# Performance work log

Hardware: AMD Instinct MI355X
Metric: run time of the kernel (lower is better)

The kernel has to match this reference:

```python
import jax, jax.numpy as jnp
from jax import lax
import numpy as np

EPS = 4e-3            # geoopt float32 ball boundary eps
MAXNORM = 1.0 - EPS   # c = 1 Poincare ball


def _norm(x):
    return jnp.sqrt(jnp.maximum(jnp.sum(x * x, axis=-1, keepdims=True), 1e-15))


def expmap0(u):
    n = _norm(u)
    return jnp.tanh(n) * u / n


def projx(x):
    n = _norm(x)
    return jnp.where(n > MAXNORM, x * (MAXNORM / n), x)


def mobius_add(x, y):
    x2 = jnp.sum(x * x, -1, keepdims=True)
    y2 = jnp.sum(y * y, -1, keepdims=True)
    xy = jnp.sum(x * y, -1, keepdims=True)
    num = (1.0 + 2.0 * xy + y2) * x + (1.0 - x2) * y
    den = 1.0 + 2.0 * xy + x2 * y2
    return num / jnp.maximum(den, 1e-15)


def mamba_layer(x, inW, convW, convb, xpW, dtW, dtb, A_log, Dp, outW):
    # x: [B,T,H]; inW: [2*Din,H]; convW: [Din,K]; xpW: [R+2N,Din]; dtW: [Din,R]
    B, T, H = x.shape
    Din, N = A_log.shape
    K = convW.shape[-1]
    R = dtW.shape[-1]
    xz = jnp.einsum('bth,dh->btd', x, inW)              # [B,T,2*Din]
    xr, z = jnp.split(xz, 2, axis=-1)
    xc = lax.conv_general_dilated(jnp.transpose(xr, (0, 2, 1)), convW[:, None, :],
                                  (1,), [(K - 1, 0)], feature_group_count=Din)
    u = jax.nn.silu(jnp.transpose(xc + convb[None, :, None], (0, 2, 1)))  # [B,T,Din]
    x_dbl = jnp.einsum('btd,ed->bte', u, xpW)           # [B,T,R+2N]
    dt_r, Bm, Cm = x_dbl[..., :R], x_dbl[..., R:R + N], x_dbl[..., R + N:]
    dt = jax.nn.softplus(jnp.einsum('btr,dr->btd', dt_r, dtW) + dtb)      # [B,T,Din]
    A = -jnp.exp(A_log)                                 # [Din,N]
    dA = jnp.exp(dt[..., None] * A)                     # [B,T,Din,N]
    dBu = dt[..., None] * Bm[:, :, None, :] * u[..., None]

    def step(h, ins):
        dA_t, dBu_t, C_t = ins
        h = dA_t * h + dBu_t                            # [B,Din,N]
        return h, jnp.einsum('bdn,bn->bd', h, C_t)

    h0 = jnp.zeros((B, Din, N), x.dtype)
    _, ys = lax.scan(step, h0, (jnp.moveaxis(dA, 1, 0), jnp.moveaxis(dBu, 1, 0), jnp.moveaxis(Cm, 1, 0)))
    y = jnp.moveaxis(ys, 0, 1) + Dp * u                 # [B,T,Din]
    return jnp.einsum('btd,hd->bth', y * jax.nn.silu(z), outW)


def _encode(xs, inp_W, inp_b, in_proj_W, conv_W, conv_b, xproj_W, dt_W, dt_b, A_log, D_skip, out_W, outp_W, outp_b):
    # xs: [4,B,T,1]; params carry leading branch dim 4, then layer dim 3
    def branch(x, iW, ib, ipW, cW, cb, xpW, dW, db, Al, Dp, oW, opW, opb):
        h = jnp.einsum('bti,hi->bth', x, iW) + ib
        for l in range(ipW.shape[0]):
            h = mamba_layer(h, ipW[l], cW[l], cb[l], xpW[l], dW[l], db[l], Al[l], Dp[l], oW[l])
        return jnp.tanh(jnp.einsum('bth,eh->bte', h, opW) + opb)
    return jax.vmap(branch)(xs, inp_W, inp_b, in_proj_W, conv_W, conv_b, xproj_W, dt_W, dt_b, A_log, D_skip, out_W, outp_W, outp_b)


def setup_inputs() -> dict:
    key = jax.random.key(0)
    ks = jax.random.split(key, 24)
    Br, B, T, H, Din, N, K, R, E, L = 4, 32, 1024, 64, 128, 16, 4, 4, 32, 3

    def rn(k, shape, s=0.05):
        return jax.random.normal(k, shape, jnp.float32) * s

    A_init = jnp.log(jnp.arange(1, N + 1, dtype=jnp.float32))
    return {
        'trend': jax.random.normal(ks[0], (B, T, 1), jnp.float32),
        'seasonal_weekly': jax.random.normal(ks[1], (B, T, 1), jnp.float32),
        'seasonal_daily': jax.random.normal(ks[2], (B, T, 1), jnp.float32),
        'residual': jax.random.normal(ks[3], (B, T, 1), jnp.float32),
        'inp_W': rn(ks[4], (Br, H, 1), 0.5),
        'inp_b': rn(ks[5], (Br, H)),
        'in_proj_W': rn(ks[6], (Br, L, 2 * Din, H)),
        'conv_W': rn(ks[7], (Br, L, Din, K), 0.2),
        'conv_b': rn(ks[8], (Br, L, Din)),
        'xproj_W': rn(ks[9], (Br, L, R + 2 * N, Din)),
        'dt_W': rn(ks[10], (Br, L, Din, R), 0.2),
        'dt_b': rn(ks[11], (Br, L, Din), 0.5) - 4.0,  # softplus(dt_b) small
        'A_log': jnp.tile(A_init, (Br, L, Din, 1)) + rn(ks[12], (Br, L, Din, N), 0.01),
        'D_skip': jnp.ones((Br, L, Din), jnp.float32) + rn(ks[13], (Br, L, Din), 0.01),
        'out_W': rn(ks[14], (Br, L, H, Din)),
        'outp_W': rn(ks[15], (Br, E, H)),
        'outp_b': rn(ks[16], (Br, E)),
    }


def reference(trend, seasonal_weekly, seasonal_daily, residual, inp_W, inp_b, in_proj_W, conv_W, conv_b, xproj_W, dt_W, dt_b, A_log, D_skip, out_W, outp_W, outp_b):
    xs = jnp.stack([trend, seasonal_weekly, seasonal_daily, residual], 0)  # [4,B,T,1]
    z = _encode(xs, inp_W, inp_b, in_proj_W, conv_W, conv_b, xproj_W, dt_W, dt_b, A_log, D_skip, out_W, outp_W, outp_b)  # [4,B,T,E]
    zh = projx(expmap0(z))
    t, w, d, r = zh[0], zh[1], zh[2], zh[3]
    comb = projx(mobius_add(mobius_add(t, mobius_add(w, d)), r))
    # stacked [trend_h, weekly_h, daily_h, residual_h, combined_h]
    return jnp.stack([t, w, d, r, comb], 0)
```

## Files before the change

### kernel.cpp

```cpp
#include <hip/hip_runtime.h>
#include <math.h>

#define TT 1024
#define DIN 128
#define HH 64
#define NN 16
#define EE 32
#define LL 3
#define BB 32

__device__ __forceinline__ float siluf(float x) { return x / (1.f + __expf(-x)); }

typedef __attribute__((ext_vector_type(8))) short bf16x8;
typedef __attribute__((ext_vector_type(4))) float f32x4;

__device__ __forceinline__ void split2(float x, ushort& hi, ushort& lo) {
  unsigned u = __float_as_uint(x);
  hi = (ushort)(u >> 16);
  float rem = x - __uint_as_float((u >> 16) << 16);
  lo = (ushort)(__float_as_uint(rem) >> 16);
}

#define WXZ_N 196608
#define WXD_N 73728
#define WOUT_N 98304

__global__ __launch_bounds__(256) void k_presplit(
    const float* __restrict__ iprojW, const float* __restrict__ xprojW,
    const float* __restrict__ outW,
    ushort* __restrict__ WxzH, ushort* __restrict__ WxzL,
    ushort* __restrict__ WxdH, ushort* __restrict__ WxdL,
    ushort* __restrict__ WoH, ushort* __restrict__ WoL) {
  int idx = blockIdx.x * 256 + threadIdx.x;
  if (idx < WXZ_N) {
    ushort h, l;
    split2(iprojW[idx], h, l);
    WxzH[idx] = h; WxzL[idx] = l;
  }
  if (idx < WXD_N) {
    int k = idx & 127, r = (idx >> 7) % 48, bl = idx / (48 * 128);
    float v = (r < 36) ? xprojW[((size_t)(bl * 36 + r)) * 128 + k] : 0.f;
    ushort h, l;
    split2(v, h, l);
    WxdH[idx] = h; WxdL[idx] = l;
  }
  if (idx < WOUT_N) {
    ushort h, l;
    split2(outW[idx], h, l);
    WoH[idx] = h; WoL[idx] = l;
  }
}

__global__ __launch_bounds__(256) void k_xz(
    const float* __restrict__ x0, const float* __restrict__ x1,
    const float* __restrict__ x2, const float* __restrict__ x3,
    const float* __restrict__ h, const ushort* __restrict__ WH,
    const ushort* __restrict__ WL,
    const float* __restrict__ inpW, const float* __restrict__ inpb,
    float* __restrict__ xr, float* __restrict__ zb, int br0, int l) {
  __shared__ __align__(16) ushort Hh[64][72], Hl[64][72];
  const int tid = threadIdx.x;
  const int b  = blockIdx.y;
  const int t0 = blockIdx.x * 64;
  const int br = br0 + (b >> 5);
  const float* Hg = h + ((size_t)b * TT + t0) * HH;
  {
    const int row = tid >> 2, c0 = (tid & 3) * 16;
    float xv = 0.f;
    if (l == 0) {
      int bb = b & 31;
      const float* xp = (br == 0) ? x0 : (br == 1) ? x1 : (br == 2) ? x2 : x3;
      xv = xp[bb * TT + t0 + row];
    }
    #pragma unroll
    for (int q = 0; q < 4; ++q) {
      float4 hv;
      if (l == 0) {
        float4 w4 = *(const float4*)(inpW + br * HH + c0 + q * 4);
        float4 b4 = *(const float4*)(inpb + br * HH + c0 + q * 4);
        hv.x = xv * w4.x + b4.x; hv.y = xv * w4.y + b4.y;
        hv.z = xv * w4.z + b4.z; hv.w = xv * w4.w + b4.w;
      } else {
        hv = *(const float4*)(Hg + (size_t)row * HH + c0 + q * 4);
      }
      ushort h0,h1,h2,h3,l0,l1,l2,l3;
      split2(hv.x,h0,l0); split2(hv.y,h1,l1); split2(hv.z,h2,l2); split2(hv.w,h3,l3);
      *(ushort4*)&Hh[row][c0 + q*4] = make_ushort4(h0,h1,h2,h3);
      *(ushort4*)&Hl[row][c0 + q*4] = make_ushort4(l0,l1,l2,l3);
    }
  }
  __syncthreads();
  const int wave = tid >> 6, lane = tid & 63;
  const int quad = lane >> 4, l16 = lane & 15;
  const int nsub = (wave & 1) * 32, tsub = (wave >> 1) * 32;
  const size_t wbase = (size_t)(br * LL + l) * 256;
  for (int n0 = 0; n0 < 2 * DIN; n0 += 64) {
    f32x4 acc[2][2] = {};
    #pragma unroll
    for (int k0 = 0; k0 < 64; k0 += 32) {
      bf16x8 Ah[2], Al[2], Bh[2], Bl[2];
      #pragma unroll
      for (int i = 0; i < 2; ++i) {
        size_t ro = (wbase + n0 + nsub + i * 16 + l16) * 64 + k0 + quad * 8;
        Ah[i] = *(const bf16x8*)(WH + ro);
        Al[i] = *(const bf16x8*)(WL + ro);
        Bh[i] = *(const bf16x8*)&Hh[tsub + i*16 + l16][k0 + quad*8];
        Bl[i] = *(const bf16x8*)&Hl[tsub + i*16 + l16][k0 + quad*8];
      }
      #pragma unroll
      for (int i = 0; i < 2; ++i)
        #pragma unroll
        for (int j = 0; j < 2; ++j) {
          acc[i][j] = __builtin_amdgcn_mfma_f32_16x16x32_bf16(Ah[i], Bh[j], acc[i][j], 0, 0, 0);
          acc[i][j] = __builtin_amdgcn_mfma_f32_16x16x32_bf16(Ah[i], Bl[j], acc[i][j], 0, 0, 0);
          acc[i][j] = __builtin_amdgcn_mfma_f32_16x16x32_bf16(Al[i], Bh[j], acc[i][j], 0, 0, 0);
        }
    }
    #pragma unroll
    for (int i = 0; i < 2; ++i) {
      #pragma unroll
      for (int r = 0; r < 4; ++r) {
        int n = n0 + nsub + i*16 + quad*4 + r;
        float* dst = (n < DIN) ? (xr + ((size_t)b * DIN + n) * TT)
                               : (zb + ((size_t)b * DIN + (n - DIN)) * TT);
        #pragma unroll
        for (int j = 0; j < 2; ++j)
          dst[t0 + tsub + j*16 + l16] = acc[i][j][r];
      }
    }
  }
}

__global__ __launch_bounds__(256) void k_xds(
    const float* __restrict__ xr, const float* __restrict__ convW,
    const float* __restrict__ convb, const ushort* __restrict__ WH,
    const ushort* __restrict__ WL, const float* __restrict__ dtW,
    const float* __restrict__ dtb, const float* __restrict__ A_log,
    const float* __restrict__ D_skip,
    float* __restrict__ cd, float* __restrict__ Cm,
    float* __restrict__ Hloc, float* __restrict__ g, float* __restrict__ sdt,
    int br0, int l) {
  __shared__ __align__(16) float U[128][66];
  __shared__ __align__(16) float Xs[40][68];
  const int tid = threadIdx.x;
  const int b  = blockIdx.y;
  const int c  = blockIdx.x;
  const int t0 = c * 64;
  const int br = br0 + (b >> 5);
  const int wave = tid >> 6, lane = tid & 63;
  const int quad = lane >> 4, l16 = lane & 15;
  const int tw = wave * 16;
  const size_t wb48 = (size_t)(br * LL + l) * 48 * 128;
  const int dd = tid >> 1, p = tid & 1;
  {
    const int tb = t0 + p * 32;
    const float* src = xr + ((size_t)b * DIN + dd) * TT + tb;
    float r[36];
    #pragma unroll
    for (int q = 0; q < 9; ++q) {
      float4 f = make_float4(0.f, 0.f, 0.f, 0.f);
      if (q > 0 || tb > 0) f = *(const float4*)(src - 4 + q * 4);
      r[q*4+0] = f.x; r[q*4+1] = f.y; r[q*4+2] = f.z; r[q*4+3] = f.w;
    }
    const int wb0 = (br * LL + l) * DIN + dd;
    const float* w = convW + (size_t)wb0 * 4;
    const float w0 = w[0], w1 = w[1], w2 = w[2], w3 = w[3];
    const float cb = convb[wb0];
    #pragma unroll
    for (int i = 0; i < 32; i += 2) {
      float o0 = siluf(r[i+1]*w0 + r[i+2]*w1 + r[i+3]*w2 + r[i+4]*w3 + cb);
      float o1 = siluf(r[i+2]*w0 + r[i+3]*w1 + r[i+4]*w2 + r[i+5]*w3 + cb);
      *(float2*)&U[dd][p * 32 + i] = make_float2(o0, o1);
    }
  }
  __syncthreads();
  f32x4 acc[3] = {};
  #pragma unroll
  for (int k0 = 0; k0 < DIN; k0 += 32) {
    ushort bh[8], bl[8];
    #pragma unroll
    for (int j = 0; j < 8; ++j)
      split2(U[k0 + quad * 8 + j][tw + l16], bh[j], bl[j]);
    bf16x8 Bh = *(bf16x8*)bh, Bl = *(bf16x8*)bl;
    #pragma unroll
    for (int nf = 0; nf < 3; ++nf) {
      size_t ro = wb48 + (size_t)(nf * 16 + l16) * 128 + k0 + quad * 8;
      bf16x8 Whf = *(const bf16x8*)(WH + ro);
      bf16x8 Wlf = *(const bf16x8*)(WL + ro);
      acc[nf] = __builtin_amdgcn_mfma_f32_16x16x32_bf16(Whf, Bh, acc[nf], 0, 0, 0);
      acc[nf] = __builtin_amdgcn_mfma_f32_16x16x32_bf16(Whf, Bl, acc[nf], 0, 0, 0);
      acc[nf] = __builtin_amdgcn_mfma_f32_16x16x32_bf16(Wlf, Bh, acc[nf], 0, 0, 0);
    }
  }
  #pragma unroll
  for (int nf = 0; nf < 3; ++nf) {
    #pragma unroll
    for (int r = 0; r < 4; ++r) {
      int n = nf * 16 + quad * 4 + r;
      if (n < 40) Xs[n][tw + l16] = acc[nf][r];
    }
  }
  __syncthreads();
  {
    int n = tid >> 4, i0 = (tid & 15) * 4;
    *(float4*)(Cm + ((size_t)b * NN + n) * TT + t0 + i0) = *(float4*)&Xs[20 + n][i0];
  }
  const int n0s = p * 8;
  const int wbase = (br * LL + l) * DIN + dd;
  const float* wd = dtW + (size_t)wbase * 4;
  const float w0 = wd[0], w1 = wd[1], w2 = wd[2], w3 = wd[3];
  const float bias = dtb[wbase];
  float Ac[8];
  #pragma unroll
  for (int j = 0; j < 8; ++j) Ac[j] = -__expf(A_log[(size_t)wbase * NN + n0s + j]);
  const float Dp = D_skip[wbase];
  float hst[8] = {0.f,0.f,0.f,0.f,0.f,0.f,0.f,0.f};
  float sd = 0.f;
  float* gp  = g  + ((size_t)b * DIN + dd) * TT + t0;
  float* cdp = cd + ((size_t)b * DIN + dd) * TT + t0;
  for (int t8 = 0; t8 < 64; t8 += 8) {
    float4 a0 = *(const float4*)&Xs[0][t8], a0b = *(const float4*)&Xs[0][t8 + 4];
    float4 a1 = *(const float4*)&Xs[1][t8], a1b = *(const float4*)&Xs[1][t8 + 4];
    float4 a2 = *(const float4*)&Xs[2][t8], a2b = *(const float4*)&Xs[2][t8 + 4];
    float4 a3 = *(const float4*)&Xs[3][t8], a3b = *(const float4*)&Xs[3][t8 + 4];
    float x0v[8] = {a0.x,a0.y,a0.z,a0.w,a0b.x,a0b.y,a0b.z,a0b.w};
    float x1v[8] = {a1.x,a1.y,a1.z,a1.w,a1b.x,a1b.y,a1b.z,a1b.w};
    float x2v[8] = {a2.x,a2.y,a2.z,a2.w,a2b.x,a2b.y,a2b.z,a2b.w};
    float x3v[8] = {a3.x,a3.y,a3.z,a3.w,a3b.x,a3b.y,a3b.z,a3b.w};
    float us[8];
    {
      float2 u0 = *(const float2*)&U[dd][t8];
      float2 u1 = *(const float2*)&U[dd][t8 + 2];
      float2 u2 = *(const float2*)&U[dd][t8 + 4];
      float2 u3 = *(const float2*)&U[dd][t8 + 6];
      us[0]=u0.x; us[1]=u0.y; us[2]=u1.x; us[3]=u1.y;
      us[4]=u2.x; us[5]=u2.y; us[6]=u3.x; us[7]=u3.y;
    }
    float dts[8], cds[8], du[8];
    #pragma unroll
    for (int s = 0; s < 8; ++s) {
      float sv = x0v[s]*w0 + x1v[s]*w1 + x2v[s]*w2 + x3v[s]*w3 + bias;
      float e = __expf(-fabsf(sv));
      float dtv = fmaxf(sv, 0.f) + __logf(1.f + e);
      sd += dtv;
      dts[s] = dtv;
      cds[s] = sd;
      du[s] = dtv * us[s];
    }
    float acc8[8] = {0.f,0.f,0.f,0.f,0.f,0.f,0.f,0.f};
    #pragma unroll
    for (int j = 0; j < 8; ++j) {
      int n = n0s + j;
      float2 b0 = *(const float2*)&Xs[4 + n][t8];
      float2 b1 = *(const float2*)&Xs[4 + n][t8 + 2];
      float2 b2 = *(const float2*)&Xs[4 + n][t8 + 4];
      float2 b3 = *(const float2*)&Xs[4 + n][t8 + 6];
      float2 c0 = *(const float2*)&Xs[20 + n][t8];
      float2 c1 = *(const float2*)&Xs[20 + n][t8 + 2];
      float2 c2 = *(const float2*)&Xs[20 + n][t8 + 4];
      float2 c3 = *(const float2*)&Xs[20 + n][t8 + 6];
      float Bv[8] = {b0.x,b0.y,b1.x,b1.y,b2.x,b2.y,b3.x,b3.y};
      float Cv[8] = {c0.x,c0.y,c1.x,c1.y,c2.x,c2.y,c3.x,c3.y};
      float hj = hst[j], an = Ac[j];
      #pragma unroll
      for (int s = 0; s < 8; ++s) {
        hj = __expf(dts[s] * an) * hj + du[s] * Bv[s];
        acc8[s] += hj * Cv[s];
      }
      hst[j] = hj;
    }
    #pragma unroll
    for (int s = 0; s < 8; ++s) {
      float tot = acc8[s] + __shfl_xor(acc8[s], 1, 2);
      acc8[s] = tot + Dp * us[s];
    }
    if (p == 0) {
      *(float4*)(gp + t8)      = make_float4(acc8[0], acc8[1], acc8[2], acc8[3]);
      *(float4*)(gp + t8 + 4)  = make_float4(acc8[4], acc8[5], acc8[6], acc8[7]);
      *(float4*)(cdp + t8)     = make_float4(cds[0], cds[1], cds[2], cds[3]);
      *(float4*)(cdp + t8 + 4) = make_float4(cds[4], cds[5], cds[6], cds[7]);
    }
  }
  {
    float* hp = Hloc + (((size_t)b * DIN + dd) * 16 + c) * 16 + n0s;
    *(float4*)hp       = make_float4(hst[0], hst[1], hst[2], hst[3]);
    *(float4*)(hp + 4) = make_float4(hst[4], hst[5], hst[6], hst[7]);
  }
  if (p == 0) sdt[((size_t)b * DIN + dd) * 16 + c] = sd;
}

__global__ __launch_bounds__(256) void k_scan2(
    const float* __restrict__ cdc, const float* __restrict__ Cm,
    const float* __restrict__ A_log, const float* __restrict__ Hloc,
    const float* __restrict__ sdt, float* __restrict__ g, int br0, int l) {
  __shared__ __align__(16) float Cl[16][68];
  __shared__ __align__(16) float HinL[32][16];
  const int bx  = blockIdx.x;
  const int b   = bx / 60;
  const int rem = bx % 60;
  const int c   = (rem >> 2) + 1;
  const int dq  = rem & 3;
  const int tid = threadIdx.x;
  const int br  = br0 + (b >> 5);
  {
    int row = tid >> 4, cc = (tid & 15) * 4;
    *(float4*)&Cl[row][cc] = *(const float4*)(Cm + ((size_t)b * NN + row) * TT + c * 64 + cc);
  }
  const int dloc = tid >> 3, tg = tid & 7;
  const int d  = dq * 32 + dloc;
  size_t off = ((size_t)b * DIN + d) * TT + c * 64 + tg * 8;
  float* gp = g + off;
  float4 y0 = *(const float4*)gp;
  float4 y1 = *(const float4*)(gp + 4);
  float4 cq0 = *(const float4*)(cdc + off);
  float4 cq1 = *(const float4*)(cdc + off + 4);
  {
    int n0 = (tid & 7) * 2;
    int wbase = (br * LL + l) * DIN + d;
    float a0 = -__expf(A_log[(size_t)wbase * NN + n0]);
    float a1 = -__expf(A_log[(size_t)wbase * NN + n0 + 1]);
    float h0 = 0.f, h1 = 0.f;
    const float* sp  = sdt + ((size_t)b * DIN + d) * 16;
    const float* hlb = Hloc + ((size_t)b * DIN + d) * 256;
    for (int cc = 0; cc < c; ++cc) {
      float sdv = sp[cc];
      float2 hl = *(const float2*)(hlb + cc * 16 + n0);
      h0 = __expf(a0 * sdv) * h0 + hl.x;
      h1 = __expf(a1 * sdv) * h1 + hl.y;
    }
    HinL[dloc][n0] = h0;
    HinL[dloc][n0 + 1] = h1;
  }
  __syncthreads();
  float cd8[8] = {cq0.x, cq0.y, cq0.z, cq0.w, cq1.x, cq1.y, cq1.z, cq1.w};
  const float* al = A_log + (size_t)((br * LL + l) * DIN + d) * NN;
  float Ac16[16];
  #pragma unroll
  for (int n = 0; n < 16; ++n) Ac16[n] = -__expf(al[n]);
  float y8[8] = {y0.x, y0.y, y0.z, y0.w, y1.x, y1.y, y1.z, y1.w};
  const int tbase = tg * 8;
  #pragma unroll
  for (int n = 0; n < 16; ++n) {
    float hv = HinL[dloc][n];
    float an = Ac16[n];
    #pragma unroll
    for (int s = 0; s < 8; ++s)
      y8[s] += Cl[n][tbase + s] * __expf(an * cd8[s]) * hv;
  }
  *(float4*)gp       = make_float4(y8[0], y8[1], y8[2], y8[3]);
  *(float4*)(gp + 4) = make_float4(y8[4], y8[5], y8[6], y8[7]);
}

__global__ __launch_bounds__(256) void k_out(
    const float* __restrict__ graw, const float* __restrict__ zb,
    const ushort* __restrict__ WH, const ushort* __restrict__ WL,
    float* __restrict__ h, int br0, int l) {
  __shared__ __align__(16) ushort Bh_[64][72], Bl_[64][72];
  const int tid = threadIdx.x;
  const int b  = blockIdx.y;
  const int t0 = blockIdx.x * 64;
  const int br = br0 + (b >> 5);
  const int wave = tid >> 6, lane = tid & 63;
  const int quad = lane >> 4, l16 = lane & 15;
  const int hsub = (wave & 1) * 32, tsub = (wave >> 1) * 32;
  const size_t wb = (size_t)(br * LL + l) * 64;
  f32x4 acc[2][2] = {};
  for (int k0 = 0; k0 < DIN; k0 += 64) {
    __syncthreads();
    {
      int row = tid >> 2, c0 = (tid & 3) * 16;
      #pragma unroll
      for (int q = 0; q < 4; ++q) {
        size_t off = ((size_t)b * DIN + k0 + row) * TT + t0 + c0 + q * 4;
        float4 gv = *(const float4*)(graw + off);
        float4 zv = *(const float4*)(zb + off);
        float a0 = gv.x * siluf(zv.x), a1 = gv.y * siluf(zv.y);
        float a2 = gv.z * siluf(zv.z), a3 = gv.w * siluf(zv.w);
        ushort h0,h1,h2,h3,l0,l1,l2,l3;
        split2(a0,h0,l0); split2(a1,h1,l1); split2(a2,h2,l2); split2(a3,h3,l3);
        *(ushort4*)&Bh_[row][c0 + q*4] = make_ushort4(h0,h1,h2,h3);
        *(ushort4*)&Bl_[row][c0 + q*4] = make_ushort4(l0,l1,l2,l3);
      }
    }
    __syncthreads();
    #pragma unroll
    for (int kk = 0; kk < 64; kk += 32) {
      bf16x8 Ahf[2], Alf[2], Bhf[2], Blf[2];
      #pragma unroll
      for (int i = 0; i < 2; ++i) {
        size_t ro = (wb + hsub + i * 16 + l16) * 128 + k0 + kk + quad * 8;
        Ahf[i] = *(const bf16x8*)(WH + ro);
        Alf[i] = *(const bf16x8*)(WL + ro);
        Bhf[i] = *(const bf16x8*)&Bh_[tsub + i*16 + l16][kk + quad*8];
        Blf[i] = *(const bf16x8*)&Bl_[tsub + i*16 + l16][kk + quad*8];
      }
      #pragma unroll
      for (int i = 0; i < 2; ++i)
        #pragma unroll
        for (int j = 0; j < 2; ++j) {
          acc[i][j] = __builtin_amdgcn_mfma_f32_16x16x32_bf16(Ahf[i], Bhf[j], acc[i][j], 0, 0, 0);
          acc[i][j] = __builtin_amdgcn_mfma_f32_16x16x32_bf16(Ahf[i], Blf[j], acc[i][j], 0, 0, 0);
          acc[i][j] = __builtin_amdgcn_mfma_f32_16x16x32_bf16(Alf[i], Bhf[j], acc[i][j], 0, 0, 0);
        }
    }
  }
  #pragma unroll
  for (int i = 0; i < 2; ++i) {
    int hh0 = hsub + i*16 + quad*4;
    #pragma unroll
    for (int j = 0; j < 2; ++j) {
      int t = t0 + tsub + j*16 + l16;
      *(f32x4*)(h + ((size_t)b * TT + t) * HH + hh0) = acc[i][j];
    }
  }
}

__global__ __launch_bounds__(256) void k_ze(
    const float* __restrict__ h, const float* __restrict__ outpW,
    const float* __restrict__ outpb, float* __restrict__ ze, int br0) {
  __shared__ __align__(16) float As[16][132];
  __shared__ __align__(16) float Ws[16][36];
  __shared__ __align__(16) float Cs[128][36];
  const int tid = threadIdx.x;
  const int b  = blockIdx.y;
  const int t0 = blockIdx.x * 128;
  const int br = br0 + (b >> 5);
  const float* W = outpW + (size_t)br * EE * HH;
  float acc[4][4] = {};
  const int ti = tid & 31, ni = tid >> 5;
  for (int k0 = 0; k0 < HH; k0 += 16) {
    __syncthreads();
    {
      int i = tid >> 1, kq = (tid & 1) * 8;
      const float* src = h + ((size_t)b * TT + t0 + i) * HH + k0 + kq;
      float4 a0 = *(const float4*)src;
      float4 a1 = *(const float4*)(src + 4);
      As[kq+0][i]=a0.x; As[kq+1][i]=a0.y; As[kq+2][i]=a0.z; As[kq+3][i]=a0.w;
      As[kq+4][i]=a1.x; As[kq+5][i]=a1.y; As[kq+6][i]=a1.z; As[kq+7][i]=a1.w;
    }
    for (int idx = tid; idx < 512; idx += 256) {
      int jj = idx >> 4, kk = idx & 15;
      Ws[kk][jj] = W[(size_t)jj * HH + k0 + kk];
    }
    __syncthreads();
    #pragma unroll
    for (int kk = 0; kk < 16; ++kk) {
      float4 a = *(const float4*)&As[kk][ti * 4];
      float4 w = *(const float4*)&Ws[kk][ni * 4];
      acc[0][0] += a.x*w.x; acc[0][1] += a.x*w.y; acc[0][2] += a.x*w.z; acc[0][3] += a.x*w.w;
      acc[1][0] += a.y*w.x; acc[1][1] += a.y*w.y; acc[1][2] += a.y*w.z; acc[1][3] += a.y*w.w;
      acc[2][0] += a.z*w.x; acc[2][1] += a.z*w.y; acc[2][2] += a.z*w.z; acc[2][3] += a.z*w.w;
      acc[3][0] += a.w*w.x; acc[3][1] += a.w*w.y; acc[3][2] += a.w*w.z; acc[3][3] += a.w*w.w;
    }
  }
  __syncthreads();
  float bj[4];
  #pragma unroll
  for (int c = 0; c < 4; ++c) bj[c] = outpb[br * EE + ni*4 + c];
  #pragma unroll
  for (int r = 0; r < 4; ++r)
    #pragma unroll
    for (int c = 0; c < 4; ++c)
      Cs[ti*4+r][ni*4+c] = tanhf(acc[r][c] + bj[c]);
  __syncthreads();
  int i = tid >> 1, j16 = (tid & 1) * 16;
  float* dst = ze + (((size_t)(br0 * 32 + b)) * TT + t0 + i) * EE + j16;
  #pragma unroll
  for (int q = 0; q < 4; ++q)
    *(float4*)(dst + q*4) = *(float4*)&Cs[i][j16 + q*4];
}

__device__ __forceinline__ void mobius_add32(const float* x, const float* y, float* o) {
  float x2 = 0.f, y2 = 0.f, xy = 0.f;
  #pragma unroll
  for (int i = 0; i < 32; ++i) { x2 += x[i]*x[i]; y2 += y[i]*y[i]; xy += x[i]*y[i]; }
  float ca  = 1.f + 2.f*xy + y2;
  float cb  = 1.f - x2;
  float den = 1.f + 2.f*xy + x2*y2;
  float inv = 1.f / fmaxf(den, 1e-15f);
  #pragma unroll
  for (int i = 0; i < 32; ++i) o[i] = (ca*x[i] + cb*y[i]) * inv;
}

__global__ __launch_bounds__(256) void k_hyper(const float* __restrict__ ze,
                                               float* __restrict__ out) {
  int idx = blockIdx.x * 256 + threadIdx.x;
  int b = idx >> 10, t = idx & 1023;
  float v[4][32];
  #pragma unroll
  for (int br = 0; br < 4; ++br) {
    const float* p = ze + (((size_t)br * BB + b) * TT + t) * EE;
    float s = 0.f;
    #pragma unroll
    for (int e = 0; e < 32; ++e) { v[br][e] = p[e]; s += v[br][e]*v[br][e]; }
    float nr = sqrtf(fmaxf(s, 1e-15f));
    float sc = tanhf(nr) / nr;
    float s2 = 0.f;
    #pragma unroll
    for (int e = 0; e < 32; ++e) { v[br][e] *= sc; s2 += v[br][e]*v[br][e]; }
    float n2 = sqrtf(fmaxf(s2, 1e-15f));
    if (n2 > 0.996f) {
      float sc2 = 0.996f / n2;
      #pragma unroll
      for (int e = 0; e < 32; ++e) v[br][e] *= sc2;
    }
    float* o = out + (((size_t)br * BB + b) * TT + t) * EE;
    #pragma unroll
    for (int e = 0; e < 32; ++e) o[e] = v[br][e];
  }
  float m1[32], m2[32];
  mobius_add32(v[1], v[2], m1);
  mobius_add32(v[0], m1, m2);
  mobius_add32(m2, v[3], m1);
  float s = 0.f;
  #pragma unroll
  for (int e = 0; e < 32; ++e) s += m1[e]*m1[e];
  float n = sqrtf(fmaxf(s, 1e-15f));
  if (n > 0.996f) {
    float sc = 0.996f / n;
    #pragma unroll
    for (int e = 0; e < 32; ++e) m1[e] *= sc;
  }
  float* o = out + (((size_t)4 * BB + b) * TT + t) * EE;
  #pragma unroll
  for (int e = 0; e < 32; ++e) o[e] = m1[e];
}

extern "C" void kernel_launch(void* const* d_in, const int* in_sizes, int n_in,
                              void* d_out, int out_size, void* d_ws, size_t ws_size,
                              hipStream_t stream) {
  const float* xs0 = (const float*)d_in[0];
  const float* xs1 = (const float*)d_in[1];
  const float* xs2 = (const float*)d_in[2];
  const float* xs3 = (const float*)d_in[3];
  const float* inpW   = (const float*)d_in[4];
  const float* inpb   = (const float*)d_in[5];
  const float* iprojW = (const float*)d_in[6];
  const float* convW  = (const float*)d_in[7];
  const float* convb  = (const float*)d_in[8];
  const float* xprojW = (const float*)d_in[9];
  const float* dtW    = (const float*)d_in[10];
  const float* dtb    = (const float*)d_in[11];
  const float* A_log  = (const float*)d_in[12];
  const float* D_skip = (const float*)d_in[13];
  const float* outW   = (const float*)d_in[14];
  const float* outpW  = (const float*)d_in[15];
  const float* outpb  = (const float*)d_in[16];
  float* out = (float*)d_out;

  const size_t wUshorts = 2 * (WXZ_N + WXD_N + WOUT_N);
  ushort* WxzH = (ushort*)d_ws;
  ushort* WxzL = WxzH + WXZ_N;
  ushort* WxdH = WxzL + WXZ_N;
  ushort* WxdL = WxdH + WXD_N;
  ushort* WoH  = WxdL + WXD_N;
  ushort* WoL  = WoH + WOUT_N;
  float* ws = (float*)(WoL + WOUT_N);

  const size_t zeF = (size_t)4 * BB * TT * EE;
  const size_t perBl = 65536 + 4 * 131072 + 2 * 16384 + 2048;
  auto needBytes = [&](int NB) {
    return (zeF + (size_t)NB * 32 * perBl) * 4 + wUshorts * 2;
  };
  int NB = 4;
  if (needBytes(4) > ws_size) NB = 2;
  if (NB == 2 && needBytes(2) > ws_size) NB = 1;
  const int nbl = NB * 32;

  float* ze = ws;
  float* h  = ze + zeF;
  float* xr = h  + (size_t)nbl * 65536;
  float* zb = xr + (size_t)nbl * 131072;
  float* g  = zb + (size_t)nbl * 131072;
  float* cd = g  + (size_t)nbl * 131072;
  float* Bm = cd + (size_t)nbl * 131072;
  float* Cm = Bm + (size_t)nbl * 16384;
  float* sdt = Cm + (size_t)nbl * 16384;
  float* Hloc = h;
  (void)Bm;

  k_presplit<<<WXZ_N / 256, 256, 0, stream>>>(iprojW, xprojW, outW,
                                              WxzH, WxzL, WxdH, WxdL, WoH, WoL);

  for (int br0 = 0; br0 < 4; br0 += NB) {
    for (int l = 0; l < LL; ++l) {
      k_xz   <<<dim3(16, nbl), 256, 0, stream>>>(xs0, xs1, xs2, xs3, h,
                                                 WxzH, WxzL, inpW, inpb, xr, zb, br0, l);
      k_xds  <<<dim3(16, nbl), 256, 0, stream>>>(xr, convW, convb, WxdH, WxdL,
                                                 dtW, dtb, A_log, D_skip,
                                                 cd, Cm, Hloc, g, sdt, br0, l);
      k_scan2<<<nbl * 60, 256, 0, stream>>>(cd, Cm, A_log, Hloc, sdt, g, br0, l);
      k_out  <<<dim3(16, nbl), 256, 0, stream>>>(g, zb, WoH, WoL, h, br0, l);
    }
    k_ze<<<dim3(8, nbl), 256, 0, stream>>>(h, outpW, outpb, ze, br0);
  }
  k_hyper<<<BB * TT / 256, 256, 0, stream>>>(ze, out);
}
```

Before: 1.005 ms.

## Fuse out-projection with next layer's in-projection to skip h round trip

```diff
diff --git a/kernel.cpp b/kernel.cpp
--- a/kernel.cpp
+++ b/kernel.cpp
@@ -251,16 +251,12 @@
     #pragma unroll
     for (int j = 0; j < 8; ++j) {
       int n = n0s + j;
-      float2 b0 = *(const float2*)&Xs[4 + n][t8];
-      float2 b1 = *(const float2*)&Xs[4 + n][t8 + 2];
-      float2 b2 = *(const float2*)&Xs[4 + n][t8 + 4];
-      float2 b3 = *(const float2*)&Xs[4 + n][t8 + 6];
-      float2 c0 = *(const float2*)&Xs[20 + n][t8];
-      float2 c1 = *(const float2*)&Xs[20 + n][t8 + 2];
-      float2 c2 = *(const float2*)&Xs[20 + n][t8 + 4];
-      float2 c3 = *(const float2*)&Xs[20 + n][t8 + 6];
-      float Bv[8] = {b0.x,b0.y,b1.x,b1.y,b2.x,b2.y,b3.x,b3.y};
-      float Cv[8] = {c0.x,c0.y,c1.x,c1.y,c2.x,c2.y,c3.x,c3.y};
+      float4 bq0 = *(const float4*)&Xs[4 + n][t8];
+      float4 bq1 = *(const float4*)&Xs[4 + n][t8 + 4];
+      float4 cq0 = *(const float4*)&Xs[20 + n][t8];
+      float4 cq1 = *(const float4*)&Xs[20 + n][t8 + 4];
+      float Bv[8] = {bq0.x,bq0.y,bq0.z,bq0.w,bq1.x,bq1.y,bq1.z,bq1.w};
+      float Cv[8] = {cq0.x,cq0.y,cq0.z,cq0.w,cq1.x,cq1.y,cq1.z,cq1.w};
       float hj = hst[j], an = Ac[j];
       #pragma unroll
       for (int s = 0; s < 8; ++s) {
@@ -349,6 +345,116 @@
   }
   *(float4*)gp       = make_float4(y8[0], y8[1], y8[2], y8[3]);
   *(float4*)(gp + 4) = make_float4(y8[4], y8[5], y8[6], y8[7]);
+}
+
+__global__ __launch_bounds__(256) void k_outxz(
+    const float* __restrict__ graw, float* zb,
+    const ushort* __restrict__ WoHp, const ushort* __restrict__ WoLp,
+    const ushort* __restrict__ WxHp, const ushort* __restrict__ WxLp,
+    float* __restrict__ xr, int br0, int l) {
+  __shared__ __align__(16) ushort Bh_[64][72], Bl_[64][72];
+  const int tid = threadIdx.x;
+  const int b  = blockIdx.y;
+  const int t0 = blockIdx.x * 64;
+  const int br = br0 + (b >> 5);
+  const int wave = tid >> 6, lane = tid & 63;
+  const int quad = lane >> 4, l16 = lane & 15;
+  const int hsub = (wave & 1) * 32, tsub = (wave >> 1) * 32;
+  const size_t wbo = (size_t)(br * LL + l) * 64;
+  f32x4 acc[2][2] = {};
+  for (int k0 = 0; k0 < DIN; k0 += 64) {
+    __syncthreads();
+    {
+      int row = tid >> 2, c0 = (tid & 3) * 16;
+      #pragma unroll
+      for (int q = 0; q < 4; ++q) {
+        size_t off = ((size_t)b * DIN + k0 + row) * TT + t0 + c0 + q * 4;
+        float4 gv = *(const float4*)(graw + off);
+        float4 zv = *(const float4*)(zb + off);
+        float a0 = gv.x * siluf(zv.x), a1 = gv.y * siluf(zv.y);
+        float a2 = gv.z * siluf(zv.z), a3 = gv.w * siluf(zv.w);
+        ushort h0,h1,h2,h3,l0,l1,l2,l3;
+        split2(a0,h0,l0); split2(a1,h1,l1); split2(a2,h2,l2); split2(a3,h3,l3);
+        *(ushort4*)&Bh_[row][c0 + q*4] = make_ushort4(h0,h1,h2,h3);
+        *(ushort4*)&Bl_[row][c0 + q*4] = make_ushort4(l0,l1,l2,l3);
+      }
+    }
+    __syncthreads();
+    #pragma unroll
+    for (int kk = 0; kk < 64; kk += 32) {
+      bf16x8 Ahf[2], Alf[2], Bhf[2], Blf[2];
+      #pragma unroll
+      for (int i = 0; i < 2; ++i) {
+        size_t ro = (wbo + hsub + i * 16 + l16) * 128 + k0 + kk + quad * 8;
+        Ahf[i] = *(const bf16x8*)(WoHp + ro);
+        Alf[i] = *(const bf16x8*)(WoLp + ro);
+        Bhf[i] = *(const bf16x8*)&Bh_[tsub + i*16 + l16][kk + quad*8];
+        Blf[i] = *(const bf16x8*)&Bl_[tsub + i*16 + l16][kk + quad*8];
+      }
+      #pragma unroll
+      for (int i = 0; i < 2; ++i)
+        #pragma unroll
+        for (int j = 0; j < 2; ++j) {
+          acc[i][j] = __builtin_amdgcn_mfma_f32_16x16x32_bf16(Ahf[i], Bhf[j], acc[i][j], 0, 0, 0);
+          acc[i][j] = __builtin_amdgcn_mfma_f32_16x16x32_bf16(Ahf[i], Blf[j], acc[i][j], 0, 0, 0);
+          acc[i][j] = __builtin_amdgcn_mfma_f32_16x16x32_bf16(Alf[i], Bhf[j], acc[i][j], 0, 0, 0);
+        }
+    }
+  }
+  __syncthreads();
+  #pragma unroll
+  for (int i = 0; i < 2; ++i) {
+    int hh0 = hsub + i*16 + quad*4;
+    #pragma unroll
+    for (int j = 0; j < 2; ++j) {
+      int t = tsub + j*16 + l16;
+      ushort h0,h1,h2,h3,l0,l1,l2,l3;
+      split2(acc[i][j][0],h0,l0); split2(acc[i][j][1],h1,l1);
+      split2(acc[i][j][2],h2,l2); split2(acc[i][j][3],h3,l3);
+      *(ushort2*)&Bh_[t][hh0]     = make_ushort2(h0,h1);
+      *(ushort2*)&Bh_[t][hh0 + 2] = make_ushort2(h2,h3);
+      *(ushort2*)&Bl_[t][hh0]     = make_ushort2(l0,l1);
+      *(ushort2*)&Bl_[t][hh0 + 2] = make_ushort2(l2,l3);
+    }
+  }
+  __syncthreads();
+  const size_t wbase = (size_t)(br * LL + (l + 1)) * 256;
+  const int nsub = hsub;
+  for (int n0 = 0; n0 < 2 * DIN; n0 += 64) {
+    f32x4 a2[2][2] = {};
+    #pragma unroll
+    for (int k0 = 0; k0 < 64; k0 += 32) {
+      bf16x8 Ah[2], Al[2], Bh[2], Bl[2];
+      #pragma unroll
+      for (int i = 0; i < 2; ++i) {
+        size_t ro = (wbase + n0 + nsub + i * 16 + l16) * 64 + k0 + quad * 8;
+        Ah[i] = *(const bf16x8*)(WxHp + ro);
+        Al[i] = *(const bf16x8*)(WxLp + ro);
+        Bh[i] = *(const bf16x8*)&Bh_[tsub + i*16 + l16][k0 + quad*8];
+        Bl[i] = *(const bf16x8*)&Bl_[tsub + i*16 + l16][k0 + quad*8];
+      }
+      #pragma unroll
+      for (int i = 0; i < 2; ++i)
+        #pragma unroll
+        for (int j = 0; j < 2; ++j) {
+          a2[i][j] = __builtin_amdgcn_mfma_f32_16x16x32_bf16(Ah[i], Bh[j], a2[i][j], 0, 0, 0);
+          a2[i][j] = __builtin_amdgcn_mfma_f32_16x16x32_bf16(Ah[i], Bl[j], a2[i][j], 0, 0, 0);
+          a2[i][j] = __builtin_amdgcn_mfma_f32_16x16x32_bf16(Al[i], Bh[j], a2[i][j], 0, 0, 0);
+        }
+    }
+    #pragma unroll
+    for (int i = 0; i < 2; ++i) {
+      #pragma unroll
+      for (int r = 0; r < 4; ++r) {
+        int n = n0 + nsub + i*16 + quad*4 + r;
+        float* dst = (n < DIN) ? (xr + ((size_t)b * DIN + n) * TT)
+                               : (zb + ((size_t)b * DIN + (n - DIN)) * TT);
+        #pragma unroll
+        for (int j = 0; j < 2; ++j)
+          dst[t0 + tsub + j*16 + l16] = a2[i][j][r];
+      }
+    }
+  }
 }
 
 __global__ __launch_bounds__(256) void k_out(
@@ -584,13 +690,18 @@
 
   for (int br0 = 0; br0 < 4; br0 += NB) {
     for (int l = 0; l < LL; ++l) {
-      k_xz   <<<dim3(16, nbl), 256, 0, stream>>>(xs0, xs1, xs2, xs3, h,
-                                                 WxzH, WxzL, inpW, inpb, xr, zb, br0, l);
+      if (l == 0)
+        k_xz<<<dim3(16, nbl), 256, 0, stream>>>(xs0, xs1, xs2, xs3, h,
+                                                WxzH, WxzL, inpW, inpb, xr, zb, br0, 0);
       k_xds  <<<dim3(16, nbl), 256, 0, stream>>>(xr, convW, convb, WxdH, WxdL,
                                                  dtW, dtb, A_log, D_skip,
                                                  cd, Cm, Hloc, g, sdt, br0, l);
       k_scan2<<<nbl * 60, 256, 0, stream>>>(cd, Cm, A_log, Hloc, sdt, g, br0, l);
-      k_out  <<<dim3(16, nbl), 256, 0, stream>>>(g, zb, WoH, WoL, h, br0, l);
+      if (l < LL - 1)
+        k_outxz<<<dim3(16, nbl), 256, 0, stream>>>(g, zb, WoH, WoL, WxzH, WxzL,
+                                                   xr, br0, l);
+      else
+        k_out<<<dim3(16, nbl), 256, 0, stream>>>(g, zb, WoH, WoL, h, br0, l);
     }
     k_ze<<<dim3(8, nbl), 256, 0, stream>>>(h, outpW, outpb, ze, br0);
   }
```

New measurement: 965.1 us. -4.0%, faster.
